# Performance work log

Measured on AMD Instinct MI355X. Metric: run time of the kernel, lower is better.

Reference implementation:

```python
import jax, jax.numpy as jnp
import numpy as np

EPS = 1e-5
PROJ_EPS = 1e-5
MAX_TANH_ARG = 15.0
NUM_LAYERS = 2

def _norm(x):
    return jnp.sqrt(jnp.sum(x * x, axis=-1, keepdims=True))

def log_map_zero(y):
    # Poincare ball log map at the origin: arctanh(||y||) * y / ||y||
    n = _norm(y)
    n_c = jnp.clip(n, EPS, 1.0 - PROJ_EPS)
    return jnp.arctanh(n_c) * y / jnp.maximum(n, EPS)

def exp_map_zero(v):
    # Poincare ball exp map at the origin: tanh(||v||) * v / ||v||
    n = _norm(v)
    n_c = jnp.clip(n, EPS, MAX_TANH_ARG)
    return jnp.tanh(n_c) * v / jnp.maximum(n, EPS)

def setup_inputs() -> dict:
    key = jax.random.key(0)
    k1, k2, k3, k4 = jax.random.split(key, 4)
    N, K, D = 50000, 32, 128
    # scale initial features so they lie inside the unit ball
    node_repr = jax.random.normal(k1, (N, D), dtype=jnp.float32) * 0.01
    adj_mat = jax.random.randint(k2, (N, K), 0, N, dtype=jnp.int32)
    weight = jax.random.uniform(k3, (N, K), dtype=jnp.float32)
    mask = jnp.ones((N, 1), dtype=jnp.float32)
    # learned params: one [D, D] matrix per layer (tie_weight=False, poincare)
    msg_weights = jax.random.normal(k4, (NUM_LAYERS, D, D), dtype=jnp.float32) * (1.0 / np.sqrt(D))
    return {"node_repr": node_repr, "adj_mat": adj_mat, "weight": weight,
            "mask": mask, "msg_weights": msg_weights}

def reference(node_repr, adj_mat, weight, mask, msg_weights):
    x = node_repr
    for step in range(NUM_LAYERS):
        # log map back to tangent space at origin (identity on first layer)
        x = (log_map_zero(x) if step > 0 else x) * mask
        msg = (x @ msg_weights[step]) * mask            # [N, D] dense projection
        nbr = msg[adj_mat]                              # [N, K, D] gather by adjacency
        combined = jnp.einsum('nk,nkd->nd', weight, nbr) * mask  # weighted neighbor sum (dropout p=0)
        x = exp_map_zero(combined) * mask               # back to the manifold
        x = jax.nn.relu(x) * mask                       # poincare activation
    return x
```

## Files before the change

### kernel.cpp

```cpp
#include <hip/hip_runtime.h>

#define EPS 1e-5f
#define PROJ_EPS 1e-5f
#define MAX_TANH_ARG 15.0f

typedef __bf16 bf16x8 __attribute__((ext_vector_type(8)));
typedef float f32x4 __attribute__((ext_vector_type(4)));
typedef float f32x2 __attribute__((ext_vector_type(2)));

__device__ __forceinline__ unsigned short f2bf(float f) {
  unsigned u = __builtin_bit_cast(unsigned, f);
  u += 0x7fffu + ((u >> 16) & 1u);
  return (unsigned short)(u >> 16);
}

union BF8 {
  unsigned short u[8];
  bf16x8 v;
  uint4 q;
};

__global__ __launch_bounds__(256) void prep_kernel(
    const float* __restrict__ W, const int* __restrict__ adj,
    const float* __restrict__ wgt, unsigned short* __restrict__ wpack,
    unsigned* __restrict__ edges, int nedge) {
  const int tid = blockIdx.x * 256 + threadIdx.x;
  if (tid < 4096) {
    const int l = tid & 63;
    const int s = (tid >> 6) & 3;
    const int tt = (tid >> 8) & 7;
    const int layer = tid >> 11;
    const int q2 = l >> 4;
    const int n = tt * 16 + (l & 15);
    unsigned short* dst = wpack + ((size_t)((layer * 32 + tt * 4 + s) * 64 + l)) * 8;
    const float* src = W + (size_t)layer * 16384;
#pragma unroll
    for (int j = 0; j < 8; ++j) {
      const int k = s * 32 + q2 * 8 + j;
      dst[j] = f2bf(src[(size_t)k * 128 + n]);
    }
  }
  const int e = tid - 4096;
  if (e >= 0 && e < nedge) {
    const unsigned id = (unsigned)adj[e] & 0xffffu;
    const unsigned short h = __builtin_bit_cast(unsigned short, (_Float16)wgt[e]);
    edges[e] = id | ((unsigned)h << 16);
  }
}

__global__ __launch_bounds__(256) void gemm0_kernel(
    const float* __restrict__ xf, const float* __restrict__ mask,
    const unsigned short* __restrict__ wpack, unsigned short* __restrict__ msg,
    int N, int planeBytes) {
  __shared__ unsigned short tile[64][136];
  const int lane = threadIdx.x & 63;
  const int wv = threadIdx.x >> 6;
  const int m = lane & 15;
  const int quad = lane >> 4;
  const int wbase = blockIdx.x * 64 + wv * 16;

  {
    const int r = lane >> 2;
    const int c = (lane & 3) * 32;
    const int gr = wbase + r;
    const int grc = gr < N ? gr : N - 1;
    const float4* src = (const float4*)(xf + (size_t)grc * 128 + c);
    unsigned short* drow = &tile[wv * 16 + r][c];
#pragma unroll
    for (int i = 0; i < 8; ++i) {
      const float4 p = src[i];
      drow[i * 4 + 0] = f2bf(p.x);
      drow[i * 4 + 1] = f2bf(p.y);
      drow[i * 4 + 2] = f2bf(p.z);
      drow[i * 4 + 3] = f2bf(p.w);
    }
  }

  f32x4 acc[8];
#pragma unroll
  for (int tt = 0; tt < 8; ++tt) acc[tt] = (f32x4){0.f, 0.f, 0.f, 0.f};
#pragma unroll
  for (int sk = 0; sk < 4; ++sk) {
    BF8 a;
    a.q = *(const uint4*)&tile[wv * 16 + m][sk * 32 + quad * 8];
#pragma unroll
    for (int tt = 0; tt < 8; ++tt) {
      BF8 b;
      b.q = *(const uint4*)(wpack + (size_t)((tt * 4 + sk) * 64 + lane) * 8);
      acc[tt] = __builtin_amdgcn_mfma_f32_16x16x32_bf16(a.v, b.v, acc[tt], 0, 0, 0);
    }
  }

  float sc[4];
#pragma unroll
  for (int r = 0; r < 4; ++r) {
    int rr = wbase + quad * 4 + r;
    rr = rr < N ? rr : N - 1;
    const float s = mask[rr];
    sc[r] = s * s;
  }
#pragma unroll
  for (int tt = 0; tt < 8; ++tt) {
    const int c = tt * 16 + m;
#pragma unroll
    for (int r = 0; r < 4; ++r)
      tile[wv * 16 + quad * 4 + r][c] = f2bf(acc[tt][r] * sc[r]);
  }
  const int r16 = lane >> 2;
  const int sub2 = lane & 3;
  const int grow = wbase + r16;
  if (grow < N) {
#pragma unroll
    for (int p = 0; p < 4; ++p) {
      *(uint4*)((char*)msg + (size_t)p * planeBytes + (size_t)grow * 64 + sub2 * 16) =
          *(const uint4*)((const char*)&tile[wv * 16 + r16][0] + p * 64 + sub2 * 16);
    }
  }
}

__global__ __launch_bounds__(256, 4) void gather_plane_kernel(
    const unsigned short* __restrict__ msg, const unsigned* __restrict__ edges,
    unsigned short* __restrict__ cout, float* __restrict__ scal,
    int N, int planeBytes) {
  __shared__ unsigned ep[64 * 36];
  const int t = threadIdx.x;
  const int p = blockIdx.x & 3;
  const int nbase = (blockIdx.x >> 2) * 64;

  for (int e = t; e < 64 * 32; e += 256) {
    const int node = e >> 5, k = e & 31;
    const int gn = nbase + node;
    ep[node * 36 + k] = (gn < N) ? edges[(size_t)gn * 32 + k] : 0u;
  }
  __syncthreads();

  const int node = t >> 2;
  const int sub = t & 3;
  const int gnode = nbase + node;
  const unsigned* mp = ep + node * 36;
  const char* plane = (const char*)msg + (size_t)p * planeBytes;
  const int suboff = sub * 16;

  unsigned ew[32];
#pragma unroll
  for (int i = 0; i < 8; ++i)
    *(uint4*)&ew[4 * i] = *(const uint4*)(mp + 4 * i);

  f32x2 acc[4];
#pragma unroll
  for (int d = 0; d < 4; ++d) acc[d] = (f32x2){0.f, 0.f};

  uint4 q[8], q2[8];
#pragma unroll
  for (int k = 0; k < 8; ++k)
    q[k] = *(const uint4*)(plane + ((size_t)(ew[k] & 0xffffu) * 64 + suboff));

#pragma unroll
  for (int b = 0; b < 4; ++b) {
    if (b < 3) {
#pragma unroll
      for (int k = 0; k < 8; ++k)
        q2[k] = *(const uint4*)(plane +
                                ((size_t)(ew[8 * (b + 1) + k] & 0xffffu) * 64 + suboff));
    }
#pragma unroll
    for (int k = 0; k < 8; ++k) {
      const float w = (float)__builtin_bit_cast(
          _Float16, (unsigned short)(ew[8 * b + k] >> 16));
      const f32x2 w2 = {w, w};
#pragma unroll
      for (int d = 0; d < 4; ++d) {
        const unsigned qd = (&q[k].x)[d];
        f32x2 v2;
        v2.x = __builtin_bit_cast(float, qd << 16);
        v2.y = __builtin_bit_cast(float, qd & 0xffff0000u);
        acc[d] = __builtin_elementwise_fma(v2, w2, acc[d]);
      }
    }
    if (b < 3) {
#pragma unroll
      for (int k = 0; k < 8; ++k) q[k] = q2[k];
    }
  }

  float s_all = 0.f, s_rel = 0.f;
  uint4 pk4;
  unsigned* pw = &pk4.x;
#pragma unroll
  for (int d = 0; d < 4; ++d) {
    s_all = fmaf(acc[d].x, acc[d].x, s_all);
    s_all = fmaf(acc[d].y, acc[d].y, s_all);
    const float r0 = fmaxf(acc[d].x, 0.f);
    const float r1 = fmaxf(acc[d].y, 0.f);
    s_rel = fmaf(r0, r0, s_rel);
    s_rel = fmaf(r1, r1, s_rel);
    pw[d] = (unsigned)f2bf(r0) | ((unsigned)f2bf(r1) << 16);
  }
  s_all += __shfl_xor(s_all, 1);
  s_all += __shfl_xor(s_all, 2);
  s_rel += __shfl_xor(s_rel, 1);
  s_rel += __shfl_xor(s_rel, 2);

  if (gnode < N) {
    *(uint4*)((char*)cout + (size_t)p * planeBytes + (size_t)gnode * 64 + suboff) = pk4;
    if (sub == 0)
      *(float2*)(scal + (size_t)gnode * 8 + p * 2) = make_float2(s_all, s_rel);
  }
}

__global__ __launch_bounds__(256) void gemm1_kernel(
    const unsigned short* __restrict__ cA, const float* __restrict__ scalA,
    const float* __restrict__ mask, const unsigned short* __restrict__ wpack2,
    unsigned short* __restrict__ msg, int N, int planeBytes) {
  __shared__ unsigned short tile[64][136];
  const int lane = threadIdx.x & 63;
  const int wv = threadIdx.x >> 6;
  const int m = lane & 15;
  const int quad = lane >> 4;
  const int wbase = blockIdx.x * 64 + wv * 16;
  const int row = wbase + m;
  const int rowc = row < N ? row : N - 1;

  f32x4 acc[8];
#pragma unroll
  for (int tt = 0; tt < 8; ++tt) acc[tt] = (f32x4){0.f, 0.f, 0.f, 0.f};
#pragma unroll
  for (int sk = 0; sk < 4; ++sk) {
    BF8 a;
    a.q = *(const uint4*)((const char*)cA + (size_t)sk * planeBytes +
                          (size_t)rowc * 64 + quad * 16);
#pragma unroll
    for (int tt = 0; tt < 8; ++tt) {
      BF8 b;
      b.q = *(const uint4*)(wpack2 + (size_t)((tt * 4 + sk) * 64 + lane) * 8);
      acc[tt] = __builtin_amdgcn_mfma_f32_16x16x32_bf16(a.v, b.v, acc[tt], 0, 0, 0);
    }
  }

  float sc[4];
#pragma unroll
  for (int r = 0; r < 4; ++r) {
    int rr = wbase + quad * 4 + r;
    rr = rr < N ? rr : N - 1;
    const float* s8 = scalA + (size_t)rr * 8;
    const float S_all = s8[0] + s8[2] + s8[4] + s8[6];
    const float S_rel = s8[1] + s8[3] + s8[5] + s8[7];
    const float mm = mask[rr];
    const float s2 = mm * mm * S_all;
    const float nrm = sqrtf(s2);
    const float ncl = fminf(fmaxf(nrm, EPS), MAX_TANH_ARG);
    const float f1 = tanhf(ncl) / fmaxf(nrm, EPS) * mm * mm * mm;
    const float r2 = f1 * f1 * S_rel;
    const float nr = sqrtf(r2);
    const float nc2 = fminf(fmaxf(nr, EPS), 1.0f - PROJ_EPS);
    const float ls = 0.5f * logf((1.f + nc2) / (1.f - nc2)) / fmaxf(nr, EPS);
    sc[r] = ls * mm * mm * f1;
  }
#pragma unroll
  for (int tt = 0; tt < 8; ++tt) {
    const int c = tt * 16 + m;
#pragma unroll
    for (int r = 0; r < 4; ++r)
      tile[wv * 16 + quad * 4 + r][c] = f2bf(acc[tt][r] * sc[r]);
  }
  const int r16 = lane >> 2;
  const int sub2 = lane & 3;
  const int grow = wbase + r16;
  if (grow < N) {
#pragma unroll
    for (int p = 0; p < 4; ++p) {
      *(uint4*)((char*)msg + (size_t)p * planeBytes + (size_t)grow * 64 + sub2 * 16) =
          *(const uint4*)((const char*)&tile[wv * 16 + r16][0] + p * 64 + sub2 * 16);
    }
  }
}

__global__ __launch_bounds__(256) void final_kernel(
    const unsigned short* __restrict__ cB, const float* __restrict__ scalB,
    const float* __restrict__ mask, float* __restrict__ out,
    int N, int planeBytes) {
  const int t = threadIdx.x;
  const int node = t >> 2;
  const int sub = t & 3;
  const int gnode = blockIdx.x * 64 + node;
  if (gnode >= N) return;
  const float* s8 = scalB + (size_t)gnode * 8;
  const float S_all = s8[0] + s8[2] + s8[4] + s8[6];
  const float mm = mask[gnode];
  const float s2 = mm * mm * S_all;
  const float nrm = sqrtf(s2);
  const float ncl = fminf(fmaxf(nrm, EPS), MAX_TANH_ARG);
  const float f2 = tanhf(ncl) / fmaxf(nrm, EPS) * mm * mm * mm;
#pragma unroll
  for (int p = 0; p < 4; ++p) {
    const uint4 q = *(const uint4*)((const char*)cB + (size_t)p * planeBytes +
                                    (size_t)gnode * 64 + sub * 16);
    float4 o0, o1;
    o0.x = f2 * __builtin_bit_cast(float, q.x << 16);
    o0.y = f2 * __builtin_bit_cast(float, q.x & 0xffff0000u);
    o0.z = f2 * __builtin_bit_cast(float, q.y << 16);
    o0.w = f2 * __builtin_bit_cast(float, q.y & 0xffff0000u);
    o1.x = f2 * __builtin_bit_cast(float, q.z << 16);
    o1.y = f2 * __builtin_bit_cast(float, q.z & 0xffff0000u);
    o1.z = f2 * __builtin_bit_cast(float, q.w << 16);
    o1.w = f2 * __builtin_bit_cast(float, q.w & 0xffff0000u);
    const int cb = p * 32 + sub * 8;
    *(float4*)(out + (size_t)gnode * 128 + cb) = o0;
    *(float4*)(out + (size_t)gnode * 128 + cb + 4) = o1;
  }
}

extern "C" void kernel_launch(void* const* d_in, const int* in_sizes, int n_in,
                              void* d_out, int out_size, void* d_ws, size_t ws_size,
                              hipStream_t stream) {
  const float* node = (const float*)d_in[0];
  const int* adj = (const int*)d_in[1];
  const float* wgt = (const float*)d_in[2];
  const float* mask = (const float*)d_in[3];
  const float* mw = (const float*)d_in[4];
  float* out = (float*)d_out;
  const int N = in_sizes[0] / 128;
  const int gb = (N + 63) / 64;
  const int planeBytes = gb * 64 * 64;
  const int nedge = N * 32;

  unsigned short* msg = (unsigned short*)d_out;
  unsigned* edges = (unsigned*)((char*)d_out + (size_t)4 * planeBytes);
  float* scalA = (float*)((char*)d_out + (size_t)4 * planeBytes + (size_t)nedge * 4);
  unsigned short* wpack = (unsigned short*)d_ws;
  unsigned short* cAB = (unsigned short*)((char*)d_ws + 65536);
  float* scalB = (float*)((char*)d_ws + 65536 + (size_t)4 * planeBytes);

  hipLaunchKernelGGL(prep_kernel, dim3((4096 + nedge + 255) / 256), dim3(256), 0,
                     stream, mw, adj, wgt, wpack, edges, nedge);
  hipLaunchKernelGGL(gemm0_kernel, dim3(gb), dim3(256), 0, stream,
                     node, mask, wpack, msg, N, planeBytes);
  hipLaunchKernelGGL(gather_plane_kernel, dim3(gb * 4), dim3(256), 0, stream,
                     msg, edges, cAB, scalA, N, planeBytes);
  hipLaunchKernelGGL(gemm1_kernel, dim3(gb), dim3(256), 0, stream,
                     cAB, scalA, mask, wpack + 16384, msg, N, planeBytes);
  hipLaunchKernelGGL(gather_plane_kernel, dim3(gb * 4), dim3(256), 0, stream,
                     msg, edges, cAB, scalB, N, planeBytes);
  hipLaunchKernelGGL(final_kernel, dim3(gb), dim3(256), 0, stream,
                     cAB, scalB, mask, out, N, planeBytes);
}
```

Baseline: 198.3 us.

## Fuse edge packing into gemm0 and deepen gather prefetch to 16 loads

Moves the adjacency/weight packing out of the prep kernel into gemm0, so each gemm0 block packs the 2048 edges of its own 64 nodes and prep only converts the weight matrices with 16 blocks. The gather kernel now keeps 16 outstanding neighbor loads in a rolling pipeline instead of double-buffered batches of 8, and its launch-bounds occupancy hint drops from 4 to 3 blocks to make room for the extra registers. The aim is to shorten the prep launch and give the latency-bound gather more memory-level parallelism, at the cost of higher register pressure and lower occupancy in the gather.

New measurement: 197.6 us. Within noise of the previous version (-0.3%).

```diff
diff --git a/kernel.cpp b/kernel.cpp
--- a/kernel.cpp
+++ b/kernel.cpp
@@ -21,43 +21,47 @@
 };
 
 __global__ __launch_bounds__(256) void prep_kernel(
-    const float* __restrict__ W, const int* __restrict__ adj,
-    const float* __restrict__ wgt, unsigned short* __restrict__ wpack,
-    unsigned* __restrict__ edges, int nedge) {
+    const float* __restrict__ W, unsigned short* __restrict__ wpack) {
   const int tid = blockIdx.x * 256 + threadIdx.x;
-  if (tid < 4096) {
-    const int l = tid & 63;
-    const int s = (tid >> 6) & 3;
-    const int tt = (tid >> 8) & 7;
-    const int layer = tid >> 11;
-    const int q2 = l >> 4;
-    const int n = tt * 16 + (l & 15);
-    unsigned short* dst = wpack + ((size_t)((layer * 32 + tt * 4 + s) * 64 + l)) * 8;
-    const float* src = W + (size_t)layer * 16384;
-#pragma unroll
-    for (int j = 0; j < 8; ++j) {
-      const int k = s * 32 + q2 * 8 + j;
-      dst[j] = f2bf(src[(size_t)k * 128 + n]);
-    }
-  }
-  const int e = tid - 4096;
-  if (e >= 0 && e < nedge) {
-    const unsigned id = (unsigned)adj[e] & 0xffffu;
-    const unsigned short h = __builtin_bit_cast(unsigned short, (_Float16)wgt[e]);
-    edges[e] = id | ((unsigned)h << 16);
+  if (tid >= 4096) return;
+  const int l = tid & 63;
+  const int s = (tid >> 6) & 3;
+  const int tt = (tid >> 8) & 7;
+  const int layer = tid >> 11;
+  const int q2 = l >> 4;
+  const int n = tt * 16 + (l & 15);
+  unsigned short* dst = wpack + ((size_t)((layer * 32 + tt * 4 + s) * 64 + l)) * 8;
+  const float* src = W + (size_t)layer * 16384;
+#pragma unroll
+  for (int j = 0; j < 8; ++j) {
+    const int k = s * 32 + q2 * 8 + j;
+    dst[j] = f2bf(src[(size_t)k * 128 + n]);
   }
 }
 
 __global__ __launch_bounds__(256) void gemm0_kernel(
     const float* __restrict__ xf, const float* __restrict__ mask,
     const unsigned short* __restrict__ wpack, unsigned short* __restrict__ msg,
-    int N, int planeBytes) {
+    const int* __restrict__ adj, const float* __restrict__ wgt,
+    unsigned* __restrict__ edges, int nedge, int N, int planeBytes) {
   __shared__ unsigned short tile[64][136];
-  const int lane = threadIdx.x & 63;
-  const int wv = threadIdx.x >> 6;
+  const int t = threadIdx.x;
+  const int lane = t & 63;
+  const int wv = t >> 6;
   const int m = lane & 15;
   const int quad = lane >> 4;
-  const int wbase = blockIdx.x * 64 + wv * 16;
+  const int base = blockIdx.x * 64;
+  const int wbase = base + wv * 16;
+
+#pragma unroll
+  for (int i = 0; i < 8; ++i) {
+    const int ge = base * 32 + i * 256 + t;
+    if (ge < nedge) {
+      const unsigned id = (unsigned)adj[ge] & 0xffffu;
+      const unsigned short h = __builtin_bit_cast(unsigned short, (_Float16)wgt[ge]);
+      edges[ge] = id | ((unsigned)h << 16);
+    }
+  }
 
   {
     const int r = lane >> 2;
@@ -118,7 +122,7 @@
   }
 }
 
-__global__ __launch_bounds__(256, 4) void gather_plane_kernel(
+__global__ __launch_bounds__(256, 3) void gather_plane_kernel(
     const unsigned short* __restrict__ msg, const unsigned* __restrict__ edges,
     unsigned short* __restrict__ cout, float* __restrict__ scal,
     int N, int planeBytes) {
@@ -150,36 +154,38 @@
 #pragma unroll
   for (int d = 0; d < 4; ++d) acc[d] = (f32x2){0.f, 0.f};
 
-  uint4 q[8], q2[8];
-#pragma unroll
-  for (int k = 0; k < 8; ++k)
+  uint4 q[16];
+#pragma unroll
+  for (int k = 0; k < 16; ++k)
     q[k] = *(const uint4*)(plane + ((size_t)(ew[k] & 0xffffu) * 64 + suboff));
 
 #pragma unroll
-  for (int b = 0; b < 4; ++b) {
-    if (b < 3) {
-#pragma unroll
-      for (int k = 0; k < 8; ++k)
-        q2[k] = *(const uint4*)(plane +
-                                ((size_t)(ew[8 * (b + 1) + k] & 0xffffu) * 64 + suboff));
-    }
-#pragma unroll
-    for (int k = 0; k < 8; ++k) {
-      const float w = (float)__builtin_bit_cast(
-          _Float16, (unsigned short)(ew[8 * b + k] >> 16));
-      const f32x2 w2 = {w, w};
-#pragma unroll
-      for (int d = 0; d < 4; ++d) {
-        const unsigned qd = (&q[k].x)[d];
-        f32x2 v2;
-        v2.x = __builtin_bit_cast(float, qd << 16);
-        v2.y = __builtin_bit_cast(float, qd & 0xffff0000u);
-        acc[d] = __builtin_elementwise_fma(v2, w2, acc[d]);
-      }
-    }
-    if (b < 3) {
-#pragma unroll
-      for (int k = 0; k < 8; ++k) q[k] = q2[k];
+  for (int k = 0; k < 16; ++k) {
+    const float w = (float)__builtin_bit_cast(_Float16, (unsigned short)(ew[k] >> 16));
+    const f32x2 w2 = {w, w};
+    const uint4 qq = q[k];
+    q[k] = *(const uint4*)(plane + ((size_t)(ew[16 + k] & 0xffffu) * 64 + suboff));
+#pragma unroll
+    for (int d = 0; d < 4; ++d) {
+      const unsigned qd = (&qq.x)[d];
+      f32x2 v2;
+      v2.x = __builtin_bit_cast(float, qd << 16);
+      v2.y = __builtin_bit_cast(float, qd & 0xffff0000u);
+      acc[d] = __builtin_elementwise_fma(v2, w2, acc[d]);
+    }
+  }
+#pragma unroll
+  for (int k = 0; k < 16; ++k) {
+    const float w = (float)__builtin_bit_cast(_Float16,
+                                              (unsigned short)(ew[16 + k] >> 16));
+    const f32x2 w2 = {w, w};
+#pragma unroll
+    for (int d = 0; d < 4; ++d) {
+      const unsigned qd = (&q[k].x)[d];
+      f32x2 v2;
+      v2.x = __builtin_bit_cast(float, qd << 16);
+      v2.y = __builtin_bit_cast(float, qd & 0xffff0000u);
+      acc[d] = __builtin_elementwise_fma(v2, w2, acc[d]);
     }
   }
 
@@ -331,10 +337,9 @@
   unsigned short* cAB = (unsigned short*)((char*)d_ws + 65536);
   float* scalB = (float*)((char*)d_ws + 65536 + (size_t)4 * planeBytes);
 
-  hipLaunchKernelGGL(prep_kernel, dim3((4096 + nedge + 255) / 256), dim3(256), 0,
-                     stream, mw, adj, wgt, wpack, edges, nedge);
+  hipLaunchKernelGGL(prep_kernel, dim3(16), dim3(256), 0, stream, mw, wpack);
   hipLaunchKernelGGL(gemm0_kernel, dim3(gb), dim3(256), 0, stream,
-                     node, mask, wpack, msg, N, planeBytes);
+                     node, mask, wpack, msg, adj, wgt, edges, nedge, N, planeBytes);
   hipLaunchKernelGGL(gather_plane_kernel, dim3(gb * 4), dim3(256), 0, stream,
                      msg, edges, cAB, scalA, N, planeBytes);
   hipLaunchKernelGGL(gemm1_kernel, dim3(gb), dim3(256), 0, stream,
```
